# Optimization experiments

Measured on AMD Instinct MI355X. Metric: run time of the kernel, lower is better.

Reference implementation:

```python
import jax, jax.numpy as jnp
import numpy as np

META_HIDDEN = 32


def _meta_apply(t, mw1, mb1, mw2, mb2):
    # t: [..., 3] triples; meta MLP 3 -> META_HIDDEN -> 1 (ReLU)
    h = jax.nn.relu(jnp.einsum('...k,hk->...h', t, mw1) + mb1)
    return jnp.einsum('...h,h->...', h, mw2[0]) + mb2[0]


def _meta_update_layer(v_in, w, v_out, mw1, mb1, mw2, mb2):
    # v_in: [I] (batch-0 input activations), w: [O, I], v_out: [O] (batch-0 output activations)
    # Builds the triples [v_i, w_ij, v_j] for every (i, j) pair and runs one batched meta pass.
    t = jnp.stack([
        jnp.broadcast_to(v_in[None, :], w.shape),
        w,
        jnp.broadcast_to(v_out[:, None], w.shape),
    ], axis=-1)  # [O, I, 3]
    return _meta_apply(t, mw1, mb1, mw2, mb2)  # [O, I] new weights


def setup_inputs() -> dict:
    key = jax.random.key(0)
    ks = jax.random.split(key, 12)
    I, H1, H2, O, B = 1024, 2048, 2048, 1024, 32
    def lin(kw, fan_in, fan_out):
        s = 1.0 / np.sqrt(fan_in)
        return jax.random.uniform(kw, (fan_out, fan_in), jnp.float32, -s, s)
    x = jax.random.normal(ks[0], (B, I), jnp.float32)
    w1 = lin(ks[1], I, H1); b1 = jax.random.uniform(ks[2], (H1,), jnp.float32, -1/np.sqrt(I), 1/np.sqrt(I))
    w2 = lin(ks[3], H1, H2); b2 = jax.random.uniform(ks[4], (H2,), jnp.float32, -1/np.sqrt(H1), 1/np.sqrt(H1))
    w3 = lin(ks[5], H2, O); b3 = jax.random.uniform(ks[6], (O,), jnp.float32, -1/np.sqrt(H2), 1/np.sqrt(H2))
    # meta network 3 -> META_HIDDEN -> 1
    mw1 = lin(ks[7], 3, META_HIDDEN); mb1 = jax.random.uniform(ks[8], (META_HIDDEN,), jnp.float32, -1/np.sqrt(3), 1/np.sqrt(3))
    mw2 = lin(ks[9], META_HIDDEN, 1); mb2 = jax.random.uniform(ks[10], (1,), jnp.float32, -1/np.sqrt(META_HIDDEN), 1/np.sqrt(META_HIDDEN))
    return {"x": x, "w1": w1, "b1": b1, "w2": w2, "b2": b2, "w3": w3, "b3": b3,
            "mw1": mw1, "mb1": mb1, "mw2": mw2, "mb2": mb2}


def reference(x, w1, b1, w2, b2, w3, b3, mw1, mb1, mw2, mb2):
    # Main 3-layer MLP forward (ReLU after every layer, including the last, as in the source).
    a0 = x
    a1 = jax.nn.relu(a0 @ w1.T + b1)
    a2 = jax.nn.relu(a1 @ w2.T + b2)
    out = jax.nn.relu(a2 @ w3.T + b3)
    # Per-weight meta update: original code loops over every (input, output) neuron pair of
    # each fc weight and writes meta_weight([v_i, w_ij, v_j]) back into the weight.
    # Only batch row 0 of the activations is used (impulse[i].data[0, idx]).
    nw1 = _meta_update_layer(a0[0], w1, a1[0], mw1, mb1, mw2, mb2)
    nw2 = _meta_update_layer(a1[0], w2, a2[0], mw1, mb1, mw2, mb2)
    nw3 = _meta_update_layer(a2[0], w3, out[0], mw1, mb1, mw2, mb2)
    return out, nw1, nw2, nw3
```

## Files before the change

kernel.cpp:

```cpp
#include <hip/hip_runtime.h>

#define THREADS 256

typedef float f2 __attribute__((ext_vector_type(2)));

__global__ __launch_bounds__(THREADS) void fwd_partial(
    const float* __restrict__ A, const float* __restrict__ W,
    float* __restrict__ P, int K, int O, int KL) {
  __shared__ float Wt[64][64];
  __shared__ float At[32][64];
  const int tid = threadIdx.x;
  const int obase = blockIdx.x * 64;
  const int ks = blockIdx.y;
  const int kbeg = ks * KL;
  const int kend = kbeg + KL;
  const int to = tid & 31;
  const int tb = tid >> 5;

  float acc[2][4] = {{0.f,0.f,0.f,0.f},{0.f,0.f,0.f,0.f}};

  for (int k0 = kbeg; k0 < kend; k0 += 64) {
    #pragma unroll
    for (int t = 0; t < 4; ++t) {
      const int id4 = tid + t * THREADS;
      const int r  = id4 >> 4;
      const int c4 = id4 & 15;
      const float4 v = *reinterpret_cast<const float4*>(
          &W[(size_t)(obase + r) * K + k0 + (c4 << 2)]);
      *reinterpret_cast<float4*>(&Wt[r][(c4 ^ (r & 15)) << 2]) = v;
    }
    #pragma unroll
    for (int t = 0; t < 2; ++t) {
      const int id4 = tid + t * THREADS;
      const int r  = id4 >> 4;
      const int c4 = id4 & 15;
      const float4 v = *reinterpret_cast<const float4*>(
          &A[(size_t)r * K + k0 + (c4 << 2)]);
      *reinterpret_cast<float4*>(&At[r][c4 << 2]) = v;
    }
    __syncthreads();

    #pragma unroll
    for (int kk = 0; kk < 64; kk += 4) {
      float4 wv[2], av[4];
      const int g = (((kk >> 2) ^ (to & 15)) << 2);
      wv[0] = *reinterpret_cast<const float4*>(&Wt[to][g]);
      wv[1] = *reinterpret_cast<const float4*>(&Wt[to + 32][g]);
      #pragma unroll
      for (int j = 0; j < 4; ++j)
        av[j] = *reinterpret_cast<const float4*>(&At[(tb << 2) + j][kk]);
      #pragma unroll
      for (int i = 0; i < 2; ++i) {
        #pragma unroll
        for (int j = 0; j < 4; ++j) {
          acc[i][j] = fmaf(wv[i].x, av[j].x, acc[i][j]);
          acc[i][j] = fmaf(wv[i].y, av[j].y, acc[i][j]);
          acc[i][j] = fmaf(wv[i].z, av[j].z, acc[i][j]);
          acc[i][j] = fmaf(wv[i].w, av[j].w, acc[i][j]);
        }
      }
    }
    __syncthreads();
  }

  #pragma unroll
  for (int i = 0; i < 2; ++i) {
    #pragma unroll
    for (int j = 0; j < 4; ++j) {
      const int b = (tb << 2) + j;
      const int o = obase + to + 32 * i;
      P[((size_t)ks * 32 + b) * O + o] = acc[i][j];
    }
  }
}

template<int KS, int O_SH>
__global__ __launch_bounds__(THREADS) void fwd_reduce_t(
    const float* __restrict__ P, const float* __restrict__ bias,
    float* __restrict__ C) {
  const int idx = blockIdx.x * THREADS + threadIdx.x;
  const int b = idx >> O_SH;
  const int o = idx & ((1 << O_SH) - 1);
  float s = 0.f;
  #pragma unroll
  for (int ks = 0; ks < KS; ++ks)
    s += P[((size_t)(ks * 32 + b) << O_SH) + o];
  C[idx] = fmaxf(s + bias[o], 0.f);
}

__global__ __launch_bounds__(THREADS) void meta_all(
    const float* __restrict__ w1, const float* __restrict__ w2, const float* __restrict__ w3,
    const float* __restrict__ a0, const float* __restrict__ a1, const float* __restrict__ a2,
    const float* __restrict__ a3,
    float* __restrict__ n1, float* __restrict__ n2, float* __restrict__ n3,
    const float* __restrict__ mw1, const float* __restrict__ mb1,
    const float* __restrict__ mw2, const float* __restrict__ mb2) {
  const int g = blockIdx.x * THREADS + threadIdx.x;
  const int n1c = (2048 * 1024) / 8;
  const int n2c = (2048 * 2048) / 8;

  const float* W; const float* vin; const float* vout; float* nw;
  int sh, e;
  if (g < n1c)            { W = w1; vin = a0; vout = a1; nw = n1; sh = 10; e = g; }
  else if (g < n1c + n2c) { W = w2; vin = a1; vout = a2; nw = n2; sh = 11; e = g - n1c; }
  else                    { W = w3; vin = a2; vout = a3; nw = n3; sh = 11; e = g - n1c - n2c; }

  const int base = e << 3;
  const int o = base >> sh;
  const int i0 = base & ((1 << sh) - 1);

  f2 wv[4], vv[4];
  {
    float4 t0 = *reinterpret_cast<const float4*>(&W[base]);
    float4 t1 = *reinterpret_cast<const float4*>(&W[base + 4]);
    wv[0] = (f2){t0.x, t0.y}; wv[1] = (f2){t0.z, t0.w};
    wv[2] = (f2){t1.x, t1.y}; wv[3] = (f2){t1.z, t1.w};
    float4 u0 = *reinterpret_cast<const float4*>(&vin[i0]);
    float4 u1 = *reinterpret_cast<const float4*>(&vin[i0 + 4]);
    vv[0] = (f2){u0.x, u0.y}; vv[1] = (f2){u0.z, u0.w};
    vv[2] = (f2){u1.x, u1.y}; vv[3] = (f2){u1.z, u1.w};
  }
  const float vo = vout[o];
  const float c2 = mb2[0];

  float r[32];
  #pragma unroll
  for (int j = 0; j < 32; ++j)
    r[j] = fmaf(mw1[3 * j + 2], vo, mb1[j]);

  f2 acc[4];
  #pragma unroll
  for (int p = 0; p < 4; ++p) acc[p] = (f2){c2, c2};

  const f2 zero = (f2){0.f, 0.f};
  #pragma unroll
  for (int j = 0; j < 32; ++j) {
    const float aj = mw1[3 * j];
    const float bj = mw1[3 * j + 1];
    const float mj = mw2[j];
    const f2 a2v = (f2){aj, aj};
    const f2 b2v = (f2){bj, bj};
    const f2 m2v = (f2){mj, mj};
    const f2 r2v = (f2){r[j], r[j]};
    #pragma unroll
    for (int p = 0; p < 4; ++p) {
#if __has_builtin(__builtin_elementwise_fma) && __has_builtin(__builtin_elementwise_max)
      f2 q = __builtin_elementwise_fma(a2v, vv[p], r2v);
      f2 h = __builtin_elementwise_fma(b2v, wv[p], q);
      h = __builtin_elementwise_max(h, zero);
      acc[p] = __builtin_elementwise_fma(m2v, h, acc[p]);
#else
      f2 h;
      h.x = fmaxf(fmaf(bj, wv[p].x, fmaf(aj, vv[p].x, r[j])), 0.f);
      h.y = fmaxf(fmaf(bj, wv[p].y, fmaf(aj, vv[p].y, r[j])), 0.f);
      acc[p].x = fmaf(mj, h.x, acc[p].x);
      acc[p].y = fmaf(mj, h.y, acc[p].y);
#endif
    }
  }

  float4 o0 = make_float4(acc[0].x, acc[0].y, acc[1].x, acc[1].y);
  float4 o1 = make_float4(acc[2].x, acc[2].y, acc[3].x, acc[3].y);
  *reinterpret_cast<float4*>(&nw[base])     = o0;
  *reinterpret_cast<float4*>(&nw[base + 4]) = o1;
}

extern "C" void kernel_launch(void* const* d_in, const int* in_sizes, int n_in,
                              void* d_out, int out_size, void* d_ws, size_t ws_size,
                              hipStream_t stream) {
  const float* x   = (const float*)d_in[0];
  const float* w1  = (const float*)d_in[1];
  const float* b1  = (const float*)d_in[2];
  const float* w2  = (const float*)d_in[3];
  const float* b2  = (const float*)d_in[4];
  const float* w3  = (const float*)d_in[5];
  const float* b3  = (const float*)d_in[6];
  const float* mw1 = (const float*)d_in[7];
  const float* mb1 = (const float*)d_in[8];
  const float* mw2 = (const float*)d_in[9];
  const float* mb2 = (const float*)d_in[10];

  float* out = (float*)d_out;
  float* n1  = out + 32 * 1024;
  float* n2  = n1 + 2048 * 1024;
  float* n3  = n2 + 2048 * 2048;

  float* ws   = (float*)d_ws;
  float* a1   = ws;
  float* a2   = ws + 65536;
  float* part = ws + 131072;

  fwd_partial<<<dim3(2048 / 64, 16), THREADS, 0, stream>>>(x, w1, part, 1024, 2048, 64);
  fwd_reduce_t<16, 11><<<(32 * 2048) / THREADS, THREADS, 0, stream>>>(part, b1, a1);
  fwd_partial<<<dim3(2048 / 64, 32), THREADS, 0, stream>>>(a1, w2, part, 2048, 2048, 64);
  fwd_reduce_t<32, 11><<<(32 * 2048) / THREADS, THREADS, 0, stream>>>(part, b2, a2);
  fwd_partial<<<dim3(1024 / 64, 32), THREADS, 0, stream>>>(a2, w3, part, 2048, 1024, 64);
  fwd_reduce_t<32, 10><<<(32 * 1024) / THREADS, THREADS, 0, stream>>>(part, b3, out);

  meta_all<<<4096, THREADS, 0, stream>>>(w1, w2, w3, x, a1, a2, out,
                                         n1, n2, n3, mw1, mb1, mw2, mb2);
}
```

Measured before the change: 60.77 us.

## Fuse GEMM, row-0 GEMV, reduction and meta update into combined overlapping launches

Replaces the separate forward GEMM, reduce and meta kernels with a single multi-role kernel launched six times. Each launch mixes GEMM partial tiles, a batch-row-0 GEMV that computes the activations the meta update needs, split-K reductions, and slices of the meta MLP work. Computing row 0 early through the GEMV lets the meta update overlap with the full-batch GEMMs instead of waiting for them. The GEMM also moves to larger 256-wide output tiles with an 8x8 register block and 128 threads. This adds heavy register pressure in the GEMM path and some redundant row-0 computation.

```diff
diff --git a/kernel.cpp b/kernel.cpp
--- a/kernel.cpp
+++ b/kernel.cpp
@@ -1,101 +1,17 @@
 #include <hip/hip_runtime.h>
 
-#define THREADS 256
+#define NT 128
 
 typedef float f2 __attribute__((ext_vector_type(2)));
 
-__global__ __launch_bounds__(THREADS) void fwd_partial(
-    const float* __restrict__ A, const float* __restrict__ W,
-    float* __restrict__ P, int K, int O, int KL) {
-  __shared__ float Wt[64][64];
-  __shared__ float At[32][64];
-  const int tid = threadIdx.x;
-  const int obase = blockIdx.x * 64;
-  const int ks = blockIdx.y;
-  const int kbeg = ks * KL;
-  const int kend = kbeg + KL;
-  const int to = tid & 31;
-  const int tb = tid >> 5;
-
-  float acc[2][4] = {{0.f,0.f,0.f,0.f},{0.f,0.f,0.f,0.f}};
-
-  for (int k0 = kbeg; k0 < kend; k0 += 64) {
-    #pragma unroll
-    for (int t = 0; t < 4; ++t) {
-      const int id4 = tid + t * THREADS;
-      const int r  = id4 >> 4;
-      const int c4 = id4 & 15;
-      const float4 v = *reinterpret_cast<const float4*>(
-          &W[(size_t)(obase + r) * K + k0 + (c4 << 2)]);
-      *reinterpret_cast<float4*>(&Wt[r][(c4 ^ (r & 15)) << 2]) = v;
-    }
-    #pragma unroll
-    for (int t = 0; t < 2; ++t) {
-      const int id4 = tid + t * THREADS;
-      const int r  = id4 >> 4;
-      const int c4 = id4 & 15;
-      const float4 v = *reinterpret_cast<const float4*>(
-          &A[(size_t)r * K + k0 + (c4 << 2)]);
-      *reinterpret_cast<float4*>(&At[r][c4 << 2]) = v;
-    }
-    __syncthreads();
-
-    #pragma unroll
-    for (int kk = 0; kk < 64; kk += 4) {
-      float4 wv[2], av[4];
-      const int g = (((kk >> 2) ^ (to & 15)) << 2);
-      wv[0] = *reinterpret_cast<const float4*>(&Wt[to][g]);
-      wv[1] = *reinterpret_cast<const float4*>(&Wt[to + 32][g]);
-      #pragma unroll
-      for (int j = 0; j < 4; ++j)
-        av[j] = *reinterpret_cast<const float4*>(&At[(tb << 2) + j][kk]);
-      #pragma unroll
-      for (int i = 0; i < 2; ++i) {
-        #pragma unroll
-        for (int j = 0; j < 4; ++j) {
-          acc[i][j] = fmaf(wv[i].x, av[j].x, acc[i][j]);
-          acc[i][j] = fmaf(wv[i].y, av[j].y, acc[i][j]);
-          acc[i][j] = fmaf(wv[i].z, av[j].z, acc[i][j]);
-          acc[i][j] = fmaf(wv[i].w, av[j].w, acc[i][j]);
-        }
-      }
-    }
-    __syncthreads();
-  }
-
-  #pragma unroll
-  for (int i = 0; i < 2; ++i) {
-    #pragma unroll
-    for (int j = 0; j < 4; ++j) {
-      const int b = (tb << 2) + j;
-      const int o = obase + to + 32 * i;
-      P[((size_t)ks * 32 + b) * O + o] = acc[i][j];
-    }
-  }
-}
-
-template<int KS, int O_SH>
-__global__ __launch_bounds__(THREADS) void fwd_reduce_t(
-    const float* __restrict__ P, const float* __restrict__ bias,
-    float* __restrict__ C) {
-  const int idx = blockIdx.x * THREADS + threadIdx.x;
-  const int b = idx >> O_SH;
-  const int o = idx & ((1 << O_SH) - 1);
-  float s = 0.f;
-  #pragma unroll
-  for (int ks = 0; ks < KS; ++ks)
-    s += P[((size_t)(ks * 32 + b) << O_SH) + o];
-  C[idx] = fmaxf(s + bias[o], 0.f);
-}
-
-__global__ __launch_bounds__(THREADS) void meta_all(
+__device__ __forceinline__ void meta_body(
+    int g,
     const float* __restrict__ w1, const float* __restrict__ w2, const float* __restrict__ w3,
     const float* __restrict__ a0, const float* __restrict__ a1, const float* __restrict__ a2,
     const float* __restrict__ a3,
     float* __restrict__ n1, float* __restrict__ n2, float* __restrict__ n3,
     const float* __restrict__ mw1, const float* __restrict__ mb1,
     const float* __restrict__ mw2, const float* __restrict__ mb2) {
-  const int g = blockIdx.x * THREADS + threadIdx.x;
   const int n1c = (2048 * 1024) / 8;
   const int n2c = (2048 * 2048) / 8;
 
@@ -159,10 +75,160 @@
     }
   }
 
-  float4 o0 = make_float4(acc[0].x, acc[0].y, acc[1].x, acc[1].y);
-  float4 o1 = make_float4(acc[2].x, acc[2].y, acc[3].x, acc[3].y);
-  *reinterpret_cast<float4*>(&nw[base])     = o0;
-  *reinterpret_cast<float4*>(&nw[base + 4]) = o1;
+  *reinterpret_cast<float4*>(&nw[base])     = make_float4(acc[0].x, acc[0].y, acc[1].x, acc[1].y);
+  *reinterpret_cast<float4*>(&nw[base + 4]) = make_float4(acc[2].x, acc[2].y, acc[3].x, acc[3].y);
+}
+
+__device__ __forceinline__ void gemm_body(
+    int bid, int tid,
+    const float* __restrict__ GA, const float* __restrict__ GW,
+    float* __restrict__ GP, int GK, int OTbits, int KLB, int GO,
+    float* __restrict__ Wt, float* __restrict__ At) {
+  const int otile = bid & ((1 << OTbits) - 1);
+  const int s = bid >> OTbits;
+  const int obase = otile << 8;
+  const int kbeg = s * KLB;
+  const int to = tid & 31;
+  const int tb = tid >> 5;
+
+  float acc[8][8];
+  #pragma unroll
+  for (int j = 0; j < 8; ++j)
+    #pragma unroll
+    for (int i = 0; i < 8; ++i) acc[j][i] = 0.f;
+
+  const int nch = KLB >> 5;
+  for (int c = 0; c < nch; ++c) {
+    const int kc = kbeg + (c << 5);
+    #pragma unroll
+    for (int t = 0; t < 16; ++t) {
+      const int id = tid + (t << 7);
+      const int r = id >> 3, p = id & 7;
+      const float4 v = *reinterpret_cast<const float4*>(
+          &GW[(size_t)(obase + r) * GK + kc + (p << 2)]);
+      *reinterpret_cast<float4*>(&Wt[(r << 5) + ((p ^ (r & 7)) << 2)]) = v;
+    }
+    #pragma unroll
+    for (int t = 0; t < 2; ++t) {
+      const int id = tid + (t << 7);
+      const int r = id >> 3, p = id & 7;
+      const float4 v = *reinterpret_cast<const float4*>(
+          &GA[(size_t)r * GK + kc + (p << 2)]);
+      *reinterpret_cast<float4*>(&At[(r << 5) + ((p ^ ((r >> 3) & 3)) << 2)]) = v;
+    }
+    __syncthreads();
+
+    #pragma unroll
+    for (int gq = 0; gq < 8; ++gq) {
+      float4 av[8], wv[8];
+      #pragma unroll
+      for (int j = 0; j < 8; ++j)
+        av[j] = *reinterpret_cast<const float4*>(
+            &At[((tb * 8 + j) << 5) + ((gq ^ tb) << 2)]);
+      const int wslot = (gq ^ (to & 7)) << 2;
+      #pragma unroll
+      for (int i = 0; i < 8; ++i)
+        wv[i] = *reinterpret_cast<const float4*>(
+            &Wt[((to + (i << 5)) << 5) + wslot]);
+      #pragma unroll
+      for (int j = 0; j < 8; ++j)
+        #pragma unroll
+        for (int i = 0; i < 8; ++i) {
+          acc[j][i] = fmaf(av[j].x, wv[i].x, acc[j][i]);
+          acc[j][i] = fmaf(av[j].y, wv[i].y, acc[j][i]);
+          acc[j][i] = fmaf(av[j].z, wv[i].z, acc[j][i]);
+          acc[j][i] = fmaf(av[j].w, wv[i].w, acc[j][i]);
+        }
+    }
+    __syncthreads();
+  }
+
+  float* pb = GP + (size_t)(s * 32) * GO + obase + to;
+  #pragma unroll
+  for (int j = 0; j < 8; ++j) {
+    float* pr = pb + (size_t)(tb * 8 + j) * GO;
+    #pragma unroll
+    for (int i = 0; i < 8; ++i)
+      pr[i << 5] = acc[j][i];
+  }
+}
+
+__device__ __forceinline__ void gemv_body(
+    int lbid, int tid,
+    const float* __restrict__ vX, const float* __restrict__ vW,
+    const float* __restrict__ vB, float* __restrict__ vR, int vK) {
+  const int w = tid >> 6, l = tid & 63;
+  const int obase = lbid * 8 + w * 4;
+  const int nt = vK >> 8;
+  float4 xv[8];
+  #pragma unroll 8
+  for (int t = 0; t < nt; ++t)
+    xv[t] = *reinterpret_cast<const float4*>(&vX[(l + (t << 6)) << 2]);
+  #pragma unroll
+  for (int q = 0; q < 4; ++q) {
+    const int o = obase + q;
+    const float* wr = vW + (size_t)o * vK;
+    float a = 0.f;
+    #pragma unroll 8
+    for (int t = 0; t < nt; ++t) {
+      const float4 wv = *reinterpret_cast<const float4*>(&wr[(l + (t << 6)) << 2]);
+      a = fmaf(wv.x, xv[t].x, a); a = fmaf(wv.y, xv[t].y, a);
+      a = fmaf(wv.z, xv[t].z, a); a = fmaf(wv.w, xv[t].w, a);
+    }
+    #pragma unroll
+    for (int m = 32; m >= 1; m >>= 1)
+      a += __shfl_xor(a, m, 64);
+    if (l == 0) vR[o] = fmaxf(a + vB[o], 0.f);
+  }
+}
+
+__device__ __forceinline__ void red_body(
+    int lbid, int tid, const float4* __restrict__ RP,
+    const float* __restrict__ Rb, float* __restrict__ RC, int ROlog) {
+  const int e4 = lbid * NT + tid;
+  const size_t sstride = (size_t)8 << ROlog;
+  float4 s = RP[e4];
+  #pragma unroll
+  for (int sl = 1; sl < 32; ++sl) {
+    const float4 v = RP[sstride * sl + e4];
+    s.x += v.x; s.y += v.y; s.z += v.z; s.w += v.w;
+  }
+  const int of = (e4 << 2) & ((1 << ROlog) - 1);
+  s.x = fmaxf(s.x + Rb[of], 0.f);
+  s.y = fmaxf(s.y + Rb[of + 1], 0.f);
+  s.z = fmaxf(s.z + Rb[of + 2], 0.f);
+  s.w = fmaxf(s.w + Rb[of + 3], 0.f);
+  *reinterpret_cast<float4*>(&RC[(size_t)e4 << 2]) = s;
+}
+
+template<int HG>
+__global__ __launch_bounds__(NT) void combo(
+    int nGemm, const float* GA, const float* GW, float* GP,
+    int GK, int OTbits, int KLB, int GO,
+    int nGemv, const float* vX, const float* vW, const float* vB, float* vR, int vK,
+    int nRed, const float4* RP, const float* Rb, float* RC, int ROlog,
+    int metaBase,
+    const float* w1, const float* w2, const float* w3,
+    const float* a0, const float* a1r, const float* a2r, const float* a3r,
+    float* n1, float* n2, float* n3,
+    const float* mw1, const float* mb1, const float* mw2, const float* mb2) {
+  const int bid = blockIdx.x;
+  const int tid = threadIdx.x;
+  if constexpr (HG != 0) {
+    if (bid < nGemm) {
+      __shared__ float Wt[256 * 32];
+      __shared__ float At[32 * 32];
+      gemm_body(bid, tid, GA, GW, GP, GK, OTbits, KLB, GO, Wt, At);
+      return;
+    }
+  }
+  int b = bid - nGemm;
+  if (b < nGemv) { gemv_body(b, tid, vX, vW, vB, vR, vK); return; }
+  b -= nGemv;
+  if (b < nRed) { red_body(b, tid, RP, Rb, RC, ROlog); return; }
+  b -= nRed;
+  const int g = metaBase + b * NT + tid;
+  meta_body(g, w1, w2, w3, a0, a1r, a2r, a3r, n1, n2, n3, mw1, mb1, mw2, mb2);
 }
 
 extern "C" void kernel_launch(void* const* d_in, const int* in_sizes, int n_in,
@@ -185,18 +251,46 @@
   float* n2  = n1 + 2048 * 1024;
   float* n3  = n2 + 2048 * 2048;
 
-  float* ws   = (float*)d_ws;
-  float* a1   = ws;
-  float* a2   = ws + 65536;
-  float* part = ws + 131072;
-
-  fwd_partial<<<dim3(2048 / 64, 16), THREADS, 0, stream>>>(x, w1, part, 1024, 2048, 64);
-  fwd_reduce_t<16, 11><<<(32 * 2048) / THREADS, THREADS, 0, stream>>>(part, b1, a1);
-  fwd_partial<<<dim3(2048 / 64, 32), THREADS, 0, stream>>>(a1, w2, part, 2048, 2048, 64);
-  fwd_reduce_t<32, 11><<<(32 * 2048) / THREADS, THREADS, 0, stream>>>(part, b2, a2);
-  fwd_partial<<<dim3(1024 / 64, 32), THREADS, 0, stream>>>(a2, w3, part, 2048, 1024, 64);
-  fwd_reduce_t<32, 10><<<(32 * 1024) / THREADS, THREADS, 0, stream>>>(part, b3, out);
-
-  meta_all<<<4096, THREADS, 0, stream>>>(w1, w2, w3, x, a1, a2, out,
-                                         n1, n2, n3, mw1, mb1, mw2, mb2);
-}
+  float* ws     = (float*)d_ws;
+  float* a1row  = ws;
+  float* a2row  = ws + 2048;
+  float* outrow = ws + 4096;
+  float* a1     = ws + 8192;
+  float* a2     = a1 + 65536;
+  float* P      = a2 + 65536;
+
+  #define METAARGS w1, w2, w3, x, a1row, a2row, outrow, n1, n2, n3, mw1, mb1, mw2, mb2
+
+  combo<1><<<512, NT, 0, stream>>>(
+      256, x, w1, P, 1024, 3, 32, 2048,
+      256, x, w1, b1, a1row, 1024,
+      0, nullptr, nullptr, nullptr, 0,
+      0, METAARGS);
+  combo<0><<<2432, NT, 0, stream>>>(
+      0, nullptr, nullptr, nullptr, 0, 0, 0, 0,
+      256, a1row, w2, b2, a2row, 2048,
+      128, (const float4*)P, b1, a1, 11,
+      0, METAARGS);
+  combo<1><<<2432, NT, 0, stream>>>(
+      256, a1, w2, P, 2048, 3, 64, 2048,
+      128, a2row, w3, b3, outrow, 2048,
+      0, nullptr, nullptr, nullptr, 0,
+      262144, METAARGS);
+  combo<0><<<2176, NT, 0, stream>>>(
+      0, nullptr, nullptr, nullptr, 0, 0, 0, 0,
+      0, nullptr, nullptr, nullptr, nullptr, 0,
+      128, (const float4*)P, b2, a2, 11,
+      524288, METAARGS);
+  combo<1><<<1664, NT, 0, stream>>>(
+      128, a2, w3, P, 2048, 2, 64, 1024,
+      0, nullptr, nullptr, nullptr, nullptr, 0,
+      0, nullptr, nullptr, nullptr, 0,
+      786432, METAARGS);
+  combo<0><<<576, NT, 0, stream>>>(
+      0, nullptr, nullptr, nullptr, 0, 0, 0, 0,
+      0, nullptr, nullptr, nullptr, nullptr, 0,
+      64, (const float4*)P, b3, out, 10,
+      983040, METAARGS);
+
+  #undef METAARGS
+}
```

New measurement: 75.71 us. 1.25x slower.

## Use split-bf16 MFMA GEMMs with fused last-block reduction and overlapped meta work

Applied to the files above, without the earlier changes.

Replaces the FP32 SIMT split-K GEMMs with bf16x3 MFMA GEMMs. The bf16 hi/lo split keeps near-FP32 accuracy. The separate reduce kernels are removed: an atomic counter lets the last split-K block sum the partials, apply bias and ReLU, and write activations, pre-split into bf16 hi/lo for the next layer. The meta-update blocks are appended to the later GEMM launches so they can overlap with the GEMM work, and the meta pass uses batch row 0 copies as soon as each layer is ready. The cost is extra MFMA work, a memset, atomics and threadfences, and more complex launch partitioning.

```diff
diff --git a/kernel.cpp b/kernel.cpp
--- a/kernel.cpp
+++ b/kernel.cpp
@@ -1,101 +1,39 @@
 #include <hip/hip_runtime.h>
 
-#define THREADS 256
-
+#define NT 256
+
+typedef unsigned int uint;
+typedef unsigned short ushort_t;
 typedef float f2 __attribute__((ext_vector_type(2)));
-
-__global__ __launch_bounds__(THREADS) void fwd_partial(
-    const float* __restrict__ A, const float* __restrict__ W,
-    float* __restrict__ P, int K, int O, int KL) {
-  __shared__ float Wt[64][64];
-  __shared__ float At[32][64];
-  const int tid = threadIdx.x;
-  const int obase = blockIdx.x * 64;
-  const int ks = blockIdx.y;
-  const int kbeg = ks * KL;
-  const int kend = kbeg + KL;
-  const int to = tid & 31;
-  const int tb = tid >> 5;
-
-  float acc[2][4] = {{0.f,0.f,0.f,0.f},{0.f,0.f,0.f,0.f}};
-
-  for (int k0 = kbeg; k0 < kend; k0 += 64) {
-    #pragma unroll
-    for (int t = 0; t < 4; ++t) {
-      const int id4 = tid + t * THREADS;
-      const int r  = id4 >> 4;
-      const int c4 = id4 & 15;
-      const float4 v = *reinterpret_cast<const float4*>(
-          &W[(size_t)(obase + r) * K + k0 + (c4 << 2)]);
-      *reinterpret_cast<float4*>(&Wt[r][(c4 ^ (r & 15)) << 2]) = v;
-    }
-    #pragma unroll
-    for (int t = 0; t < 2; ++t) {
-      const int id4 = tid + t * THREADS;
-      const int r  = id4 >> 4;
-      const int c4 = id4 & 15;
-      const float4 v = *reinterpret_cast<const float4*>(
-          &A[(size_t)r * K + k0 + (c4 << 2)]);
-      *reinterpret_cast<float4*>(&At[r][c4 << 2]) = v;
-    }
-    __syncthreads();
-
-    #pragma unroll
-    for (int kk = 0; kk < 64; kk += 4) {
-      float4 wv[2], av[4];
-      const int g = (((kk >> 2) ^ (to & 15)) << 2);
-      wv[0] = *reinterpret_cast<const float4*>(&Wt[to][g]);
-      wv[1] = *reinterpret_cast<const float4*>(&Wt[to + 32][g]);
-      #pragma unroll
-      for (int j = 0; j < 4; ++j)
-        av[j] = *reinterpret_cast<const float4*>(&At[(tb << 2) + j][kk]);
-      #pragma unroll
-      for (int i = 0; i < 2; ++i) {
-        #pragma unroll
-        for (int j = 0; j < 4; ++j) {
-          acc[i][j] = fmaf(wv[i].x, av[j].x, acc[i][j]);
-          acc[i][j] = fmaf(wv[i].y, av[j].y, acc[i][j]);
-          acc[i][j] = fmaf(wv[i].z, av[j].z, acc[i][j]);
-          acc[i][j] = fmaf(wv[i].w, av[j].w, acc[i][j]);
-        }
-      }
-    }
-    __syncthreads();
-  }
-
-  #pragma unroll
-  for (int i = 0; i < 2; ++i) {
-    #pragma unroll
-    for (int j = 0; j < 4; ++j) {
-      const int b = (tb << 2) + j;
-      const int o = obase + to + 32 * i;
-      P[((size_t)ks * 32 + b) * O + o] = acc[i][j];
-    }
-  }
-}
-
-template<int KS, int O_SH>
-__global__ __launch_bounds__(THREADS) void fwd_reduce_t(
-    const float* __restrict__ P, const float* __restrict__ bias,
-    float* __restrict__ C) {
-  const int idx = blockIdx.x * THREADS + threadIdx.x;
-  const int b = idx >> O_SH;
-  const int o = idx & ((1 << O_SH) - 1);
-  float s = 0.f;
-  #pragma unroll
-  for (int ks = 0; ks < KS; ++ks)
-    s += P[((size_t)(ks * 32 + b) << O_SH) + o];
-  C[idx] = fmaxf(s + bias[o], 0.f);
-}
-
-__global__ __launch_bounds__(THREADS) void meta_all(
+typedef short bh8 __attribute__((ext_vector_type(8)));
+typedef float f32x4 __attribute__((ext_vector_type(4)));
+typedef uint u32x4 __attribute__((ext_vector_type(4)));
+
+__device__ __forceinline__ uint hi2(float a, float b) {
+  return (__float_as_uint(a) >> 16) | (__float_as_uint(b) & 0xffff0000u);
+}
+__device__ __forceinline__ uint lo2(float a, float b) {
+  const float r0 = a - __uint_as_float(__float_as_uint(a) & 0xffff0000u);
+  const float r1 = b - __uint_as_float(__float_as_uint(b) & 0xffff0000u);
+  return hi2(r0, r1);
+}
+__device__ __forceinline__ void split8(const float* __restrict__ s, bh8& hi, bh8& lo) {
+  const float4 v0 = *reinterpret_cast<const float4*>(s);
+  const float4 v1 = *reinterpret_cast<const float4*>(s + 4);
+  u32x4 h = {hi2(v0.x, v0.y), hi2(v0.z, v0.w), hi2(v1.x, v1.y), hi2(v1.z, v1.w)};
+  u32x4 t = {lo2(v0.x, v0.y), lo2(v0.z, v0.w), lo2(v1.x, v1.y), lo2(v1.z, v1.w)};
+  hi = __builtin_bit_cast(bh8, h);
+  lo = __builtin_bit_cast(bh8, t);
+}
+
+__device__ __forceinline__ void meta_body(
+    int g,
     const float* __restrict__ w1, const float* __restrict__ w2, const float* __restrict__ w3,
     const float* __restrict__ a0, const float* __restrict__ a1, const float* __restrict__ a2,
     const float* __restrict__ a3,
     float* __restrict__ n1, float* __restrict__ n2, float* __restrict__ n3,
     const float* __restrict__ mw1, const float* __restrict__ mb1,
     const float* __restrict__ mw2, const float* __restrict__ mb2) {
-  const int g = blockIdx.x * THREADS + threadIdx.x;
   const int n1c = (2048 * 1024) / 8;
   const int n2c = (2048 * 2048) / 8;
 
@@ -159,10 +97,128 @@
     }
   }
 
-  float4 o0 = make_float4(acc[0].x, acc[0].y, acc[1].x, acc[1].y);
-  float4 o1 = make_float4(acc[2].x, acc[2].y, acc[3].x, acc[3].y);
-  *reinterpret_cast<float4*>(&nw[base])     = o0;
-  *reinterpret_cast<float4*>(&nw[base + 4]) = o1;
+  *reinterpret_cast<float4*>(&nw[base])     = make_float4(acc[0].x, acc[0].y, acc[1].x, acc[1].y);
+  *reinterpret_cast<float4*>(&nw[base + 4]) = make_float4(acc[2].x, acc[2].y, acc[3].x, acc[3].y);
+}
+
+template<int MODE>
+__device__ __forceinline__ void winner_reduce(
+    int ob, int tid, const float* __restrict__ P, const float* __restrict__ bias,
+    int O, ushort_t* __restrict__ aHi, ushort_t* __restrict__ aLo,
+    float* __restrict__ row0, float* __restrict__ outF) {
+  const int o0 = (ob << 7) + ((tid & 63) << 1);
+  const int bg = tid >> 6;
+  #pragma unroll
+  for (int bb = 0; bb < 8; ++bb) {
+    const int b = bg * 8 + bb;
+    float s0 = 0.f, s1 = 0.f;
+    #pragma unroll
+    for (int sl = 0; sl < 16; ++sl) {
+      const f2 v = *reinterpret_cast<const f2*>(&P[((size_t)sl * 32 + b) * O + o0]);
+      s0 += v.x; s1 += v.y;
+    }
+    const float v0 = fmaxf(s0 + bias[o0], 0.f);
+    const float v1 = fmaxf(s1 + bias[o0 + 1], 0.f);
+    if constexpr (MODE == 0) {
+      reinterpret_cast<uint*>(aHi)[((size_t)b * O + o0) >> 1] = hi2(v0, v1);
+      reinterpret_cast<uint*>(aLo)[((size_t)b * O + o0) >> 1] = lo2(v0, v1);
+      if (b == 0) *reinterpret_cast<f2*>(&row0[o0]) = (f2){v0, v1};
+    } else {
+      *reinterpret_cast<f2*>(&outF[(size_t)b * O + o0]) = (f2){v0, v1};
+    }
+  }
+}
+
+template<int KL, int OBL, int AF32, int MODE>
+__device__ __forceinline__ void gemm_fwd(
+    int gb, int tid,
+    const float* __restrict__ Af32, const ushort_t* __restrict__ Ahi,
+    const ushort_t* __restrict__ Alo,
+    const float* __restrict__ W, int K, int O,
+    float* __restrict__ P, int* __restrict__ cnt, const float* __restrict__ bias,
+    ushort_t* __restrict__ nHi, ushort_t* __restrict__ nLo,
+    float* __restrict__ row0, float* __restrict__ outF) {
+  const int ob = gb & ((1 << OBL) - 1);
+  const int sl = gb >> OBL;
+  const int w = tid >> 6, l = tid & 63;
+  const int l15 = l & 15, lk = l >> 4;
+  const int b0 = (w & 1) << 4;
+  const int obw = (ob << 7) + ((w >> 1) << 6);
+  const int kbeg = sl * KL;
+  const int bA = b0 + l15;
+
+  f32x4 acc[4];
+  #pragma unroll
+  for (int of = 0; of < 4; ++of)
+    #pragma unroll
+    for (int e = 0; e < 4; ++e) acc[of][e] = 0.f;
+
+  #pragma unroll
+  for (int st = 0; st < KL / 32; ++st) {
+    const int kk = kbeg + (st << 5) + (lk << 3);
+    bh8 ahi, alo;
+    if constexpr (AF32) {
+      split8(&Af32[(size_t)bA * K + kk], ahi, alo);
+    } else {
+      ahi = *reinterpret_cast<const bh8*>(&Ahi[(size_t)bA * K + kk]);
+      alo = *reinterpret_cast<const bh8*>(&Alo[(size_t)bA * K + kk]);
+    }
+    #pragma unroll
+    for (int of = 0; of < 4; ++of) {
+      const int ow = obw + (of << 4) + l15;
+      bh8 whi, wlo;
+      split8(&W[(size_t)ow * K + kk], whi, wlo);
+      acc[of] = __builtin_amdgcn_mfma_f32_16x16x32_bf16(ahi, whi, acc[of], 0, 0, 0);
+      acc[of] = __builtin_amdgcn_mfma_f32_16x16x32_bf16(ahi, wlo, acc[of], 0, 0, 0);
+      acc[of] = __builtin_amdgcn_mfma_f32_16x16x32_bf16(alo, whi, acc[of], 0, 0, 0);
+    }
+  }
+
+  #pragma unroll
+  for (int of = 0; of < 4; ++of) {
+    const int o = obw + (of << 4) + l15;
+    #pragma unroll
+    for (int r = 0; r < 4; ++r) {
+      const int b = b0 + lk * 4 + r;
+      P[((size_t)sl * 32 + b) * O + o] = acc[of][r];
+    }
+  }
+
+  __shared__ int flag;
+  __syncthreads();
+  if (tid == 0) {
+    __threadfence();
+    const int old = __hip_atomic_fetch_add(&cnt[ob], 1, __ATOMIC_ACQ_REL,
+                                           __HIP_MEMORY_SCOPE_AGENT);
+    flag = (old == 15);
+  }
+  __syncthreads();
+  if (flag) {
+    __threadfence();
+    winner_reduce<MODE>(ob, tid, P, bias, O, nHi, nLo, row0, outF);
+  }
+}
+
+template<int KL, int OBL, int AF32, int MODE>
+__global__ __launch_bounds__(NT) void stepk(
+    int nGemm,
+    const float* Af32, const ushort_t* Ahi, const ushort_t* Alo,
+    const float* W, int K, int O,
+    float* P, int* cnt, const float* bias,
+    ushort_t* nHi, ushort_t* nLo, float* row0, float* outF,
+    int mStart,
+    const float* w1, const float* w2, const float* w3,
+    const float* a0, const float* a1r, const float* a2r, const float* a3r,
+    float* n1, float* n2, float* n3,
+    const float* mw1, const float* mb1, const float* mw2, const float* mb2) {
+  const int bid = blockIdx.x;
+  if (bid < nGemm) {
+    gemm_fwd<KL, OBL, AF32, MODE>(bid, threadIdx.x, Af32, Ahi, Alo, W, K, O,
+                                  P, cnt, bias, nHi, nLo, row0, outF);
+    return;
+  }
+  const int g = mStart + (bid - nGemm) * NT + threadIdx.x;
+  meta_body(g, w1, w2, w3, a0, a1r, a2r, a3r, n1, n2, n3, mw1, mb1, mw2, mb2);
 }
 
 extern "C" void kernel_launch(void* const* d_in, const int* in_sizes, int n_in,
@@ -185,18 +241,35 @@
   float* n2  = n1 + 2048 * 1024;
   float* n3  = n2 + 2048 * 2048;
 
-  float* ws   = (float*)d_ws;
-  float* a1   = ws;
-  float* a2   = ws + 65536;
-  float* part = ws + 131072;
-
-  fwd_partial<<<dim3(2048 / 64, 16), THREADS, 0, stream>>>(x, w1, part, 1024, 2048, 64);
-  fwd_reduce_t<16, 11><<<(32 * 2048) / THREADS, THREADS, 0, stream>>>(part, b1, a1);
-  fwd_partial<<<dim3(2048 / 64, 32), THREADS, 0, stream>>>(a1, w2, part, 2048, 2048, 64);
-  fwd_reduce_t<32, 11><<<(32 * 2048) / THREADS, THREADS, 0, stream>>>(part, b2, a2);
-  fwd_partial<<<dim3(1024 / 64, 32), THREADS, 0, stream>>>(a2, w3, part, 2048, 1024, 64);
-  fwd_reduce_t<32, 10><<<(32 * 1024) / THREADS, THREADS, 0, stream>>>(part, b3, out);
-
-  meta_all<<<4096, THREADS, 0, stream>>>(w1, w2, w3, x, a1, a2, out,
-                                         n1, n2, n3, mw1, mb1, mw2, mb2);
-}
+  float* ws = (float*)d_ws;
+  int*   cnt   = (int*)ws;
+  float* row01 = ws + 64;
+  float* row02 = row01 + 2048;
+  ushort_t* a1hi = (ushort_t*)(row02 + 2048);
+  ushort_t* a1lo = a1hi + 65536;
+  ushort_t* a2hi = a1lo + 65536;
+  ushort_t* a2lo = a2hi + 65536;
+  float* P = (float*)(a2lo + 65536);
+
+  #define MARGS w1, w2, w3, x, row01, row02, out, n1, n2, n3, mw1, mb1, mw2, mb2
+
+  hipMemsetAsync(cnt, 0, 40 * sizeof(int), stream);
+
+  stepk<64, 4, 1, 0><<<256, NT, 0, stream>>>(
+      256, x, nullptr, nullptr, w1, 1024, 2048,
+      P, cnt + 0, b1, a1hi, a1lo, row01, nullptr, 0, MARGS);
+
+  stepk<128, 4, 0, 0><<<256 + 1024, NT, 0, stream>>>(
+      256, nullptr, a1hi, a1lo, w2, 2048, 2048,
+      P, cnt + 16, b2, a2hi, a2lo, row02, nullptr, 0, MARGS);
+
+  stepk<128, 3, 0, 1><<<128 + 2048, NT, 0, stream>>>(
+      128, nullptr, a2hi, a2lo, w3, 2048, 1024,
+      P, cnt + 32, b3, nullptr, nullptr, nullptr, out, 262144, MARGS);
+
+  stepk<128, 3, 0, 1><<<1024, NT, 0, stream>>>(
+      0, nullptr, nullptr, nullptr, nullptr, 0, 0,
+      nullptr, nullptr, nullptr, nullptr, nullptr, nullptr, nullptr, 786432, MARGS);
+
+  #undef MARGS
+}
```

Result: slower. 101.5 us (+67.0%).
